# Kernel tuning notes

Hardware: AMD Instinct MI355X
Metric: run time of the kernel (lower is better)

Reference implementation:

```python
import jax, jax.numpy as jnp
import numpy as np

B, D, C = 8192, 1024, 4096  # batch, d_model, num_clusters (all active)
EPS = 1e-12  # matches F.normalize eps


def _l2_normalize(x):
    n = jnp.linalg.norm(x, axis=-1, keepdims=True)
    return x / jnp.maximum(n, EPS)


def setup_inputs() -> dict:
    key = jax.random.key(0)
    k1, k2 = jax.random.split(key)
    embedding = jax.random.normal(k1, (B, D), dtype=jnp.float32)
    centroids = jax.random.normal(k2, (C, D), dtype=jnp.float32)  # buffer, all active
    return {"embedding": embedding, "centroids": centroids}


def reference(embedding, centroids):
    # Fused equivalent of the per-centroid Python loop:
    # cosine sim of normalized embedding vs each normalized centroid.
    emb_n = _l2_normalize(embedding)        # [B, D]
    cen_n = _l2_normalize(centroids)        # [C, D]
    sims = jnp.clip(emb_n @ cen_n.T, 0.0, 1.0)  # [B, C], per-sim clamp to [0,1]
    max_sim = jnp.max(sims, axis=-1)        # [B]
    closest = jnp.argmax(sims, axis=-1)     # [B] int
    novelty = jnp.clip(jnp.sqrt(1.0 - max_sim), 0.0, 1.0)  # [B]
    return novelty, closest
```

## Files before the change

### kernel.cpp

```cpp
#include <hip/hip_runtime.h>
#include <math.h>

#define B_ROWS 8192
#define C_COLS 4096
#define D_DIM  1024
#define EPSN   1e-12f

typedef float v4f __attribute__((ext_vector_type(4)));
typedef short v8s __attribute__((ext_vector_type(8)));

__device__ __forceinline__ unsigned short bf16_rtn(float x) {
    unsigned int u = __float_as_uint(x);
    u += 0x7fffu + ((u >> 16) & 1u);
    return (unsigned short)(u >> 16);
}

__device__ __forceinline__ bool better_vi(float v, int i, float V, int I) {
    return (v > V) || (v == V && i < I);
}

__global__ __launch_bounds__(256) void prep_kernel(
    const float* __restrict__ emb, const float* __restrict__ cen,
    unsigned short* __restrict__ Ah, unsigned short* __restrict__ Bh,
    float* __restrict__ inv_a, float* __restrict__ inv_b)
{
    const int lane = threadIdx.x & 63;
    const int wid  = blockIdx.x * 4 + (threadIdx.x >> 6);
    const float* src; unsigned short* dst; float* invp; int r;
    if (wid < B_ROWS) { src = emb; r = wid;          dst = Ah; invp = inv_a; }
    else              { src = cen; r = wid - B_ROWS; dst = Bh; invp = inv_b; }

    const float* rp = src + (size_t)r * D_DIM;
    float4 v[4];
    float ss = 0.0f;
    #pragma unroll
    for (int j = 0; j < 4; ++j) {
        v[j] = *(const float4*)(rp + (j * 64 + lane) * 4);
        ss += v[j].x * v[j].x + v[j].y * v[j].y + v[j].z * v[j].z + v[j].w * v[j].w;
    }
    #pragma unroll
    for (int off = 1; off < 64; off <<= 1) ss += __shfl_xor(ss, off, 64);

    const float iv = 1.0f / fmaxf(sqrtf(ss), EPSN);
    if (lane == 0) invp[r] = iv;

    unsigned short* dp = dst + (size_t)r * D_DIM;
    #pragma unroll
    for (int j = 0; j < 4; ++j) {
        ushort4 H;
        H.x = bf16_rtn(v[j].x * iv);
        H.y = bf16_rtn(v[j].y * iv);
        H.z = bf16_rtn(v[j].z * iv);
        H.w = bf16_rtn(v[j].w * iv);
        *(ushort4*)(dp + (j * 64 + lane) * 4) = H;
    }
}

__global__ __launch_bounds__(256, 4) void simmax_kernel(
    const unsigned short* __restrict__ Ahg, const unsigned short* __restrict__ Bhg,
    float* __restrict__ p1v, int* __restrict__ p1i,
    float* __restrict__ p2v, int* __restrict__ p2i)
{
    __shared__ unsigned short lds[2 * 8192];

    const int tid    = threadIdx.x;
    const int L      = tid & 63;
    const int w      = tid >> 6;
    const int lane15 = L & 15;
    const int quad   = L >> 4;
    const int wr     = w >> 1, wc = w & 1;
    const int row0   = blockIdx.x * 128;
    const int c0     = blockIdx.y * 128;

    const int scol = (tid & 7) ^ ((tid >> 3) & 7);
    const unsigned short* aBase = Ahg + (size_t)(row0 + (tid >> 3)) * D_DIM + scol * 8;
    const unsigned short* bBase = Bhg + (size_t)(c0   + (tid >> 3)) * D_DIM + scol * 8;

    v4f acc[4][4];
    #pragma unroll
    for (int mt = 0; mt < 4; ++mt)
        #pragma unroll
        for (int nt = 0; nt < 4; ++nt) acc[mt][nt] = (v4f)0.0f;

    int rAo[4], rBo[4];
    #pragma unroll
    for (int t = 0; t < 4; ++t) {
        rAo[t] = (wr * 64 + t * 16 + lane15) * 64;
        rBo[t] = (wc * 64 + t * 16 + lane15) * 64;
    }
    const int s7 = lane15 & 7;
    const int cq[2] = { (quad ^ s7) * 8, ((4 + quad) ^ s7) * 8 };

    for (int kc = 0; kc < D_DIM / 64; ++kc) {
        const int kb = kc * 64;
        #pragma unroll
        for (int i = 0; i < 4; ++i) {
            __builtin_amdgcn_global_load_lds(
                (const __attribute__((address_space(1))) void*)(aBase + (size_t)i * 32 * D_DIM + kb),
                (__attribute__((address_space(3))) void*)&lds[(i * 256 + w * 64) * 8], 16, 0, 0);
            __builtin_amdgcn_global_load_lds(
                (const __attribute__((address_space(1))) void*)(bBase + (size_t)i * 32 * D_DIM + kb),
                (__attribute__((address_space(3))) void*)&lds[8192 + (i * 256 + w * 64) * 8], 16, 0, 0);
        }
        __syncthreads();

        #pragma unroll
        for (int h = 0; h < 2; ++h) {
            v8s fah[4], fbh[4];
            #pragma unroll
            for (int t = 0; t < 4; ++t) {
                fah[t] = *(const v8s*)&lds[rAo[t] + cq[h]];
                fbh[t] = *(const v8s*)&lds[8192 + rBo[t] + cq[h]];
            }
            #pragma unroll
            for (int mt = 0; mt < 4; ++mt)
                #pragma unroll
                for (int nt = 0; nt < 4; ++nt)
                    acc[mt][nt] = __builtin_amdgcn_mfma_f32_16x16x32_bf16(fah[mt], fbh[nt], acc[mt][nt], 0, 0, 0);
        }
        __syncthreads();
    }

    const int pc = blockIdx.y * 2 + wc;
    #pragma unroll
    for (int mt = 0; mt < 4; ++mt) {
        #pragma unroll
        for (int r = 0; r < 4; ++r) {
            float a1v = acc[mt][0][r];
            int   a1i = c0 + wc * 64 + 0 * 16 + lane15;
            float a2v = -1e30f;
            int   a2i = 0x7fffffff;
            #pragma unroll
            for (int nt = 1; nt < 4; ++nt) {
                float v  = acc[mt][nt][r];
                int   ci = c0 + wc * 64 + nt * 16 + lane15;
                if (better_vi(v, ci, a1v, a1i))      { a2v = a1v; a2i = a1i; a1v = v; a1i = ci; }
                else if (better_vi(v, ci, a2v, a2i)) { a2v = v;   a2i = ci; }
            }
            #pragma unroll
            for (int off = 8; off; off >>= 1) {
                float b1v = __shfl_down(a1v, off, 64); int b1i = __shfl_down(a1i, off, 64);
                float b2v = __shfl_down(a2v, off, 64); int b2i = __shfl_down(a2i, off, 64);
                if (better_vi(b1v, b1i, a1v, a1i)) {
                    if (better_vi(a1v, a1i, b2v, b2i)) { a2v = a1v; a2i = a1i; }
                    else                               { a2v = b2v; a2i = b2i; }
                    a1v = b1v; a1i = b1i;
                } else if (better_vi(b1v, b1i, a2v, a2i)) {
                    a2v = b1v; a2i = b1i;
                }
            }
            if (lane15 == 0) {
                int rg = row0 + wr * 64 + mt * 16 + quad * 4 + r;
                size_t ix = (size_t)rg * 64 + pc;
                p1v[ix] = a1v; p1i[ix] = a1i;
                p2v[ix] = a2v; p2i[ix] = a2i;
            }
        }
    }
}

__global__ __launch_bounds__(256) void finalize_kernel(
    const float* __restrict__ emb, const float* __restrict__ cen,
    const float* __restrict__ inv_a, const float* __restrict__ inv_b,
    const float* __restrict__ p1v, const int* __restrict__ p1i,
    const float* __restrict__ p2v, const int* __restrict__ p2i,
    float* __restrict__ out)
{
    const int lane = threadIdx.x & 63;
    const int row  = blockIdx.x * 4 + (threadIdx.x >> 6);
    const size_t base = (size_t)row * 64 + lane;

    float v[4]; int ix[4];
    v[0] = p1v[base]; ix[0] = p1i[base];
    v[1] = p2v[base]; ix[1] = p2i[base];
    v[2] = -1e30f;    ix[2] = 0x7ffffffe;
    v[3] = -1e30f;    ix[3] = 0x7fffffff;

    #pragma unroll
    for (int off = 1; off < 64; off <<= 1) {
        float ov[4]; int oi[4];
        #pragma unroll
        for (int k = 0; k < 4; ++k) {
            ov[k] = __shfl_xor(v[k],  off, 64);
            oi[k] = __shfl_xor(ix[k], off, 64);
        }
        #pragma unroll
        for (int k = 0; k < 4; ++k) {
            float bv = ov[k]; int bi = oi[k];
            bool b0 = better_vi(bv, bi, v[0], ix[0]);
            bool b1 = better_vi(bv, bi, v[1], ix[1]);
            bool b2 = better_vi(bv, bi, v[2], ix[2]);
            bool b3 = better_vi(bv, bi, v[3], ix[3]);
            float nv3 = b2 ? v[2] : (b3 ? bv : v[3]); int ni3 = b2 ? ix[2] : (b3 ? bi : ix[3]);
            float nv2 = b1 ? v[1] : (b2 ? bv : v[2]); int ni2 = b1 ? ix[1] : (b2 ? bi : ix[2]);
            float nv1 = b0 ? v[0] : (b1 ? bv : v[1]); int ni1 = b0 ? ix[0] : (b1 ? bi : ix[1]);
            float nv0 = b0 ? bv   : v[0];             int ni0 = b0 ? bi    : ix[0];
            v[0] = nv0; ix[0] = ni0; v[1] = nv1; ix[1] = ni1;
            v[2] = nv2; ix[2] = ni2; v[3] = nv3; ix[3] = ni3;
        }
    }

    const float* er = emb + (size_t)row * D_DIM;
    const float* cr0 = cen + (size_t)ix[0] * D_DIM;
    const float* cr1 = cen + (size_t)ix[1] * D_DIM;
    const float* cr2 = cen + (size_t)ix[2] * D_DIM;
    const float* cr3 = cen + (size_t)ix[3] * D_DIM;

    float d[4] = { 0.0f, 0.0f, 0.0f, 0.0f };
    #pragma unroll
    for (int j = 0; j < 4; ++j) {
        int e = (j * 64 + lane) * 4;
        float4 ev = *(const float4*)(er  + e);
        float4 c0 = *(const float4*)(cr0 + e);
        float4 c1 = *(const float4*)(cr1 + e);
        float4 c2 = *(const float4*)(cr2 + e);
        float4 c3 = *(const float4*)(cr3 + e);
        d[0] += ev.x * c0.x + ev.y * c0.y + ev.z * c0.z + ev.w * c0.w;
        d[1] += ev.x * c1.x + ev.y * c1.y + ev.z * c1.z + ev.w * c1.w;
        d[2] += ev.x * c2.x + ev.y * c2.y + ev.z * c2.z + ev.w * c2.w;
        d[3] += ev.x * c3.x + ev.y * c3.y + ev.z * c3.z + ev.w * c3.w;
    }
    #pragma unroll
    for (int off = 1; off < 64; off <<= 1) {
        #pragma unroll
        for (int c = 0; c < 4; ++c) d[c] += __shfl_xor(d[c], off, 64);
    }

    if (lane == 0) {
        const float ia = inv_a[row];
        float m = -1e30f; int ci = 0x7fffffff;
        #pragma unroll
        for (int c = 0; c < 4; ++c) {
            float s = d[c] * ia * inv_b[ix[c]];
            if (better_vi(s, ix[c], m, ci)) { m = s; ci = ix[c]; }
        }
        if (m <= 0.0f) ci = 0;
        float ms = fminf(fmaxf(m, 0.0f), 1.0f);
        out[row]          = fminf(fmaxf(sqrtf(1.0f - ms), 0.0f), 1.0f);
        out[B_ROWS + row] = (float)ci;
    }
}

extern "C" void kernel_launch(void* const* d_in, const int* in_sizes, int n_in,
                              void* d_out, int out_size, void* d_ws, size_t ws_size,
                              hipStream_t stream)
{
    const float* emb = (const float*)d_in[0];
    const float* cen = (const float*)d_in[1];
    float* out = (float*)d_out;

    unsigned short* Ahp = (unsigned short*)d_ws;
    unsigned short* Bhp = Ahp + (size_t)B_ROWS * D_DIM;
    float* inv_a = (float*)(Bhp + (size_t)C_COLS * D_DIM);
    float* inv_b = inv_a + B_ROWS;
    float* p1v   = inv_b + C_COLS;
    int*   p1i   = (int*)(p1v + (size_t)64 * B_ROWS);
    float* p2v   = (float*)(p1i + (size_t)64 * B_ROWS);
    int*   p2i   = (int*)(p2v + (size_t)64 * B_ROWS);

    prep_kernel<<<(B_ROWS + C_COLS) / 4, 256, 0, stream>>>(emb, cen, Ahp, Bhp, inv_a, inv_b);

    dim3 grid(B_ROWS / 128, C_COLS / 128);
    simmax_kernel<<<grid, 256, 0, stream>>>(Ahp, Bhp, p1v, p1i, p2v, p2i);

    finalize_kernel<<<B_ROWS / 4, 256, 0, stream>>>(emb, cen, inv_a, inv_b,
                                                    p1v, p1i, p2v, p2i, out);
}
```

Baseline: 207.8 us.

## Triple-buffer GEMM loads with 512-thread 128x256 tiles and split MFMA phases

The similarity GEMM moves from 128x128 tiles with 4 waves and a single-buffered load/sync loop to 128x256 tiles with 8 waves. Global-to-LDS loads go into a three-stage ring buffer, with the prefetch for step t+2 issued in two halves interleaved with two MFMA phases. Explicit vmcnt waits, barriers and s_setprio hints are meant to hide load latency and raise MFMA utilization. In exchange it uses much more LDS (about 144 KB per block) and fewer resident blocks, and the partial-result indexing now depends on the wider column tiles.

```diff
diff --git a/kernel.cpp b/kernel.cpp
--- a/kernel.cpp
+++ b/kernel.cpp
@@ -56,25 +56,43 @@
     }
 }
 
-__global__ __launch_bounds__(256, 4) void simmax_kernel(
+#define GLD16(gp, lp) \
+    __builtin_amdgcn_global_load_lds( \
+        (const __attribute__((address_space(1))) void*)(gp), \
+        (__attribute__((address_space(3))) void*)(lp), 16, 0, 0)
+
+__global__ __launch_bounds__(512, 2) void simmax_kernel(
     const unsigned short* __restrict__ Ahg, const unsigned short* __restrict__ Bhg,
     float* __restrict__ p1v, int* __restrict__ p1i,
     float* __restrict__ p2v, int* __restrict__ p2i)
 {
-    __shared__ unsigned short lds[2 * 8192];
+    __shared__ unsigned short lds[3 * 24576];
 
     const int tid    = threadIdx.x;
     const int L      = tid & 63;
     const int w      = tid >> 6;
     const int lane15 = L & 15;
     const int quad   = L >> 4;
-    const int wr     = w >> 1, wc = w & 1;
+    const int wr     = w >> 2;
+    const int wc     = w & 3;
     const int row0   = blockIdx.x * 128;
-    const int c0     = blockIdx.y * 128;
+    const int c0     = blockIdx.y * 256;
 
     const int scol = (tid & 7) ^ ((tid >> 3) & 7);
-    const unsigned short* aBase = Ahg + (size_t)(row0 + (tid >> 3)) * D_DIM + scol * 8;
-    const unsigned short* bBase = Bhg + (size_t)(c0   + (tid >> 3)) * D_DIM + scol * 8;
+    const unsigned short* aB = Ahg + (size_t)(row0 + (tid >> 3)) * D_DIM + scol * 8;
+    const unsigned short* bB = Bhg + (size_t)(c0   + (tid >> 3)) * D_DIM + scol * 8;
+    const int wofs = w * 512;
+
+#define STAGE3A(bo, kb) do { \
+    GLD16(aB + (kb),           &lds[(bo) + wofs]);           \
+    GLD16(aB + 65536 + (kb),   &lds[(bo) + 4096  + wofs]);   \
+    GLD16(bB + (kb),           &lds[(bo) + 8192  + wofs]);   \
+} while (0)
+#define STAGE3B(bo, kb) do { \
+    GLD16(bB + 65536 + (kb),   &lds[(bo) + 12288 + wofs]);   \
+    GLD16(bB + 131072 + (kb),  &lds[(bo) + 16384 + wofs]);   \
+    GLD16(bB + 196608 + (kb),  &lds[(bo) + 20480 + wofs]);   \
+} while (0)
 
     v4f acc[4][4];
     #pragma unroll
@@ -86,42 +104,79 @@
     #pragma unroll
     for (int t = 0; t < 4; ++t) {
         rAo[t] = (wr * 64 + t * 16 + lane15) * 64;
-        rBo[t] = (wc * 64 + t * 16 + lane15) * 64;
-    }
-    const int s7 = lane15 & 7;
-    const int cq[2] = { (quad ^ s7) * 8, ((4 + quad) ^ s7) * 8 };
-
-    for (int kc = 0; kc < D_DIM / 64; ++kc) {
-        const int kb = kc * 64;
-        #pragma unroll
-        for (int i = 0; i < 4; ++i) {
-            __builtin_amdgcn_global_load_lds(
-                (const __attribute__((address_space(1))) void*)(aBase + (size_t)i * 32 * D_DIM + kb),
-                (__attribute__((address_space(3))) void*)&lds[(i * 256 + w * 64) * 8], 16, 0, 0);
-            __builtin_amdgcn_global_load_lds(
-                (const __attribute__((address_space(1))) void*)(bBase + (size_t)i * 32 * D_DIM + kb),
-                (__attribute__((address_space(3))) void*)&lds[8192 + (i * 256 + w * 64) * 8], 16, 0, 0);
-        }
-        __syncthreads();
-
-        #pragma unroll
-        for (int h = 0; h < 2; ++h) {
-            v8s fah[4], fbh[4];
+        rBo[t] = 8192 + (wc * 64 + t * 16 + lane15) * 64;
+    }
+    const int s7  = lane15 & 7;
+    const int cq0 = (quad ^ s7) * 8;
+    const int cq1 = ((4 + quad) ^ s7) * 8;
+
+    STAGE3A(0, 0);      STAGE3B(0, 0);
+    STAGE3A(24576, 64); STAGE3B(24576, 64);
+    asm volatile("s_waitcnt vmcnt(6)" ::: "memory");
+    __builtin_amdgcn_s_barrier();
+
+    int bo_c = 0, bo_n = 24576, bo_n2 = 49152;
+    for (int t = 0; t < 16; ++t) {
+        const bool pf  = (t + 2 < 16);
+        const int  kb2 = (t + 2) * 64;
+
+        v8s fb[4][2], fa[2][2];
+        #pragma unroll
+        for (int nt = 0; nt < 4; ++nt) {
+            fb[nt][0] = *(const v8s*)&lds[bo_c + rBo[nt] + cq0];
+            fb[nt][1] = *(const v8s*)&lds[bo_c + rBo[nt] + cq1];
+        }
+        #pragma unroll
+        for (int mt = 0; mt < 2; ++mt) {
+            fa[mt][0] = *(const v8s*)&lds[bo_c + rAo[mt] + cq0];
+            fa[mt][1] = *(const v8s*)&lds[bo_c + rAo[mt] + cq1];
+        }
+        if (pf) STAGE3A(bo_n2, kb2);
+        __builtin_amdgcn_s_barrier();
+        asm volatile("s_waitcnt lgkmcnt(0)" ::: "memory");
+        __builtin_amdgcn_sched_barrier(0);
+        __builtin_amdgcn_s_setprio(1);
+        #pragma unroll
+        for (int kk = 0; kk < 2; ++kk)
             #pragma unroll
-            for (int t = 0; t < 4; ++t) {
-                fah[t] = *(const v8s*)&lds[rAo[t] + cq[h]];
-                fbh[t] = *(const v8s*)&lds[8192 + rBo[t] + cq[h]];
-            }
-            #pragma unroll
-            for (int mt = 0; mt < 4; ++mt)
+            for (int mt = 0; mt < 2; ++mt)
                 #pragma unroll
                 for (int nt = 0; nt < 4; ++nt)
-                    acc[mt][nt] = __builtin_amdgcn_mfma_f32_16x16x32_bf16(fah[mt], fbh[nt], acc[mt][nt], 0, 0, 0);
-        }
-        __syncthreads();
-    }
-
-    const int pc = blockIdx.y * 2 + wc;
+                    acc[mt][nt] = __builtin_amdgcn_mfma_f32_16x16x32_bf16(
+                        fa[mt][kk], fb[nt][kk], acc[mt][nt], 0, 0, 0);
+        __builtin_amdgcn_s_setprio(0);
+        __builtin_amdgcn_s_barrier();
+
+        v8s fa2[2][2];
+        #pragma unroll
+        for (int mt = 0; mt < 2; ++mt) {
+            fa2[mt][0] = *(const v8s*)&lds[bo_c + rAo[2 + mt] + cq0];
+            fa2[mt][1] = *(const v8s*)&lds[bo_c + rAo[2 + mt] + cq1];
+        }
+        if (pf) STAGE3B(bo_n2, kb2);
+        __builtin_amdgcn_s_barrier();
+        asm volatile("s_waitcnt lgkmcnt(0)" ::: "memory");
+        __builtin_amdgcn_sched_barrier(0);
+        __builtin_amdgcn_s_setprio(1);
+        #pragma unroll
+        for (int kk = 0; kk < 2; ++kk)
+            #pragma unroll
+            for (int mt = 0; mt < 2; ++mt)
+                #pragma unroll
+                for (int nt = 0; nt < 4; ++nt)
+                    acc[2 + mt][nt] = __builtin_amdgcn_mfma_f32_16x16x32_bf16(
+                        fa2[mt][kk], fb[nt][kk], acc[2 + mt][nt], 0, 0, 0);
+        __builtin_amdgcn_s_setprio(0);
+
+        if (t < 15) {
+            if (pf) asm volatile("s_waitcnt vmcnt(6)" ::: "memory");
+            else    asm volatile("s_waitcnt vmcnt(0)" ::: "memory");
+            __builtin_amdgcn_s_barrier();
+        }
+        const int tb = bo_c; bo_c = bo_n; bo_n = bo_n2; bo_n2 = tb;
+    }
+
+    const int pc = blockIdx.y * 4 + wc;
     #pragma unroll
     for (int mt = 0; mt < 4; ++mt) {
         #pragma unroll
@@ -260,8 +315,8 @@
 
     prep_kernel<<<(B_ROWS + C_COLS) / 4, 256, 0, stream>>>(emb, cen, Ahp, Bhp, inv_a, inv_b);
 
-    dim3 grid(B_ROWS / 128, C_COLS / 128);
-    simmax_kernel<<<grid, 256, 0, stream>>>(Ahp, Bhp, p1v, p1i, p2v, p2i);
+    dim3 grid(B_ROWS / 128, C_COLS / 256);
+    simmax_kernel<<<grid, 512, 0, stream>>>(Ahp, Bhp, p1v, p1i, p2v, p2i);
 
     finalize_kernel<<<B_ROWS / 4, 256, 0, stream>>>(emb, cen, inv_a, inv_b,
                                                     p1v, p1i, p2v, p2i, out);
```

After: 232.1 us. 1.12x slower.

## Enlarge GEMM tile to 256x256 with double-buffered LDS and swizzled block order

Applied to the files above, without the earlier changes.

The similarity GEMM kernel moves from 128x128 tiles with 4 waves to 256x256 tiles with 8 waves per block, each wave computing a 128x64 sub-tile. The K loop is now double-buffered in LDS so the next chunk's global-to-LDS loads are issued before the current chunk's MFMAs, which also removes one barrier per iteration. Block IDs are remapped into grouped tiles to improve L2 locality. The partial-argmax column index layout still yields 64 partials per row. Costs are 128KB of LDS and 128 accumulator registers per thread, which may limit occupancy.

```diff
diff --git a/kernel.cpp b/kernel.cpp
--- a/kernel.cpp
+++ b/kernel.cpp
@@ -56,74 +56,94 @@
     }
 }
 
-__global__ __launch_bounds__(256, 4) void simmax_kernel(
+#define GLD16(gp, lp) \
+    __builtin_amdgcn_global_load_lds( \
+        (const __attribute__((address_space(1))) void*)(gp), \
+        (__attribute__((address_space(3))) void*)(lp), 16, 0, 0)
+
+__global__ __launch_bounds__(512, 2) void simmax_kernel(
     const unsigned short* __restrict__ Ahg, const unsigned short* __restrict__ Bhg,
     float* __restrict__ p1v, int* __restrict__ p1i,
     float* __restrict__ p2v, int* __restrict__ p2i)
 {
-    __shared__ unsigned short lds[2 * 8192];
+    __shared__ unsigned short lds[2 * 32768];
 
     const int tid    = threadIdx.x;
     const int L      = tid & 63;
     const int w      = tid >> 6;
     const int lane15 = L & 15;
     const int quad   = L >> 4;
-    const int wr     = w >> 1, wc = w & 1;
-    const int row0   = blockIdx.x * 128;
-    const int c0     = blockIdx.y * 128;
+    const int wr     = w >> 2;
+    const int wc     = w & 3;
+
+    const int bid = blockIdx.x;
+    const int c   = bid & 7, s = bid >> 3;
+    const int gx  = ((c & 3) << 3) + (s & 7);
+    const int gy  = ((c >> 2) << 3) + (s >> 3);
+    const int row0 = gx * 256;
+    const int c0   = gy * 256;
 
     const int scol = (tid & 7) ^ ((tid >> 3) & 7);
-    const unsigned short* aBase = Ahg + (size_t)(row0 + (tid >> 3)) * D_DIM + scol * 8;
-    const unsigned short* bBase = Bhg + (size_t)(c0   + (tid >> 3)) * D_DIM + scol * 8;
-
-    v4f acc[4][4];
-    #pragma unroll
-    for (int mt = 0; mt < 4; ++mt)
+    const unsigned short* aB = Ahg + (size_t)(row0 + (tid >> 3)) * D_DIM + scol * 8;
+    const unsigned short* bB = Bhg + (size_t)(c0   + (tid >> 3)) * D_DIM + scol * 8;
+    const int wofs = w * 512;
+
+#define STAGE_ALL(bo, kb) do { \
+    GLD16(aB + (kb),           &lds[(bo) + 0     + wofs]); \
+    GLD16(aB + 65536  + (kb),  &lds[(bo) + 4096  + wofs]); \
+    GLD16(aB + 131072 + (kb),  &lds[(bo) + 8192  + wofs]); \
+    GLD16(aB + 196608 + (kb),  &lds[(bo) + 12288 + wofs]); \
+    GLD16(bB + (kb),           &lds[(bo) + 16384 + wofs]); \
+    GLD16(bB + 65536  + (kb),  &lds[(bo) + 20480 + wofs]); \
+    GLD16(bB + 131072 + (kb),  &lds[(bo) + 24576 + wofs]); \
+    GLD16(bB + 196608 + (kb),  &lds[(bo) + 28672 + wofs]); \
+} while (0)
+
+    v4f acc[8][4];
+    #pragma unroll
+    for (int mt = 0; mt < 8; ++mt)
         #pragma unroll
         for (int nt = 0; nt < 4; ++nt) acc[mt][nt] = (v4f)0.0f;
 
-    int rAo[4], rBo[4];
-    #pragma unroll
-    for (int t = 0; t < 4; ++t) {
-        rAo[t] = (wr * 64 + t * 16 + lane15) * 64;
-        rBo[t] = (wc * 64 + t * 16 + lane15) * 64;
-    }
-    const int s7 = lane15 & 7;
-    const int cq[2] = { (quad ^ s7) * 8, ((4 + quad) ^ s7) * 8 };
-
-    for (int kc = 0; kc < D_DIM / 64; ++kc) {
-        const int kb = kc * 64;
-        #pragma unroll
-        for (int i = 0; i < 4; ++i) {
-            __builtin_amdgcn_global_load_lds(
-                (const __attribute__((address_space(1))) void*)(aBase + (size_t)i * 32 * D_DIM + kb),
-                (__attribute__((address_space(3))) void*)&lds[(i * 256 + w * 64) * 8], 16, 0, 0);
-            __builtin_amdgcn_global_load_lds(
-                (const __attribute__((address_space(1))) void*)(bBase + (size_t)i * 32 * D_DIM + kb),
-                (__attribute__((address_space(3))) void*)&lds[8192 + (i * 256 + w * 64) * 8], 16, 0, 0);
-        }
-        __syncthreads();
+    int rA[8], rB[4];
+    #pragma unroll
+    for (int t = 0; t < 8; ++t) rA[t] = (wr * 128 + t * 16 + lane15) * 64;
+    #pragma unroll
+    for (int t = 0; t < 4; ++t) rB[t] = 16384 + (wc * 64 + t * 16 + lane15) * 64;
+    const int s7  = lane15 & 7;
+    const int cq0 = (quad ^ s7) * 8;
+    const int cq1 = ((4 + quad) ^ s7) * 8;
+
+    STAGE_ALL(0, 0);
+    __syncthreads();
+
+    int cur = 0;
+    for (int t = 0; t < 16; ++t) {
+        const int bo = cur << 15;
+        if (t < 15) STAGE_ALL(32768 - bo, (t + 1) * 64);
 
         #pragma unroll
         for (int h = 0; h < 2; ++h) {
-            v8s fah[4], fbh[4];
-            #pragma unroll
-            for (int t = 0; t < 4; ++t) {
-                fah[t] = *(const v8s*)&lds[rAo[t] + cq[h]];
-                fbh[t] = *(const v8s*)&lds[8192 + rBo[t] + cq[h]];
-            }
-            #pragma unroll
-            for (int mt = 0; mt < 4; ++mt)
+            const int cq = h ? cq1 : cq0;
+            v8s fb[4], fa[8];
+            #pragma unroll
+            for (int nt = 0; nt < 4; ++nt) fb[nt] = *(const v8s*)&lds[bo + rB[nt] + cq];
+            #pragma unroll
+            for (int mt = 0; mt < 8; ++mt) fa[mt] = *(const v8s*)&lds[bo + rA[mt] + cq];
+            #pragma unroll
+            for (int mt = 0; mt < 8; ++mt)
                 #pragma unroll
                 for (int nt = 0; nt < 4; ++nt)
-                    acc[mt][nt] = __builtin_amdgcn_mfma_f32_16x16x32_bf16(fah[mt], fbh[nt], acc[mt][nt], 0, 0, 0);
-        }
-        __syncthreads();
-    }
-
-    const int pc = blockIdx.y * 2 + wc;
-    #pragma unroll
-    for (int mt = 0; mt < 4; ++mt) {
+                    acc[mt][nt] = __builtin_amdgcn_mfma_f32_16x16x32_bf16(
+                        fa[mt], fb[nt], acc[mt][nt], 0, 0, 0);
+        }
+        if (t < 15) __syncthreads();
+        cur ^= 1;
+    }
+
+    const int pc = gy * 4 + wc;
+    #pragma unroll
+    for (int mt = 0; mt < 8; ++mt) {
         #pragma unroll
         for (int r = 0; r < 4; ++r) {
             float a1v = acc[mt][0][r];
@@ -150,7 +170,7 @@
                 }
             }
             if (lane15 == 0) {
-                int rg = row0 + wr * 64 + mt * 16 + quad * 4 + r;
+                int rg = row0 + wr * 128 + mt * 16 + quad * 4 + r;
                 size_t ix = (size_t)rg * 64 + pc;
                 p1v[ix] = a1v; p1i[ix] = a1i;
                 p2v[ix] = a2v; p2i[ix] = a2i;
@@ -260,8 +280,7 @@
 
     prep_kernel<<<(B_ROWS + C_COLS) / 4, 256, 0, stream>>>(emb, cen, Ahp, Bhp, inv_a, inv_b);
 
-    dim3 grid(B_ROWS / 128, C_COLS / 128);
-    simmax_kernel<<<grid, 256, 0, stream>>>(Ahp, Bhp, p1v, p1i, p2v, p2i);
+    simmax_kernel<<<dim3(512), 512, 0, stream>>>(Ahp, Bhp, p1v, p1i, p2v, p2i);
 
     finalize_kernel<<<B_ROWS / 4, 256, 0, stream>>>(emb, cen, inv_a, inv_b,
                                                     p1v, p1i, p2v, p2i, out);
```

After: 222.5 us. 1.07x slower.

## Enlarge GEMM block tile to 256x128 with 512 threads sharing B tile

Applied to the files above, without the earlier changes.

Doubles the row dimension of each simmax block to 256 rows using 8 waves, so each staged centroid tile in LDS is reused by twice as many waves. The staging code is rewritten so each thread issues six 16-byte global-to-LDS loads per K-chunk, and LDS grows to 48KB. This is meant to cut global/L2 traffic for the B operand and halve the block count. In exchange, larger blocks and more LDS per block may lower occupancy. The epilogue's per-wave indexing of partial results must also still line up with the new wave layout.

```diff
diff --git a/kernel.cpp b/kernel.cpp
--- a/kernel.cpp
+++ b/kernel.cpp
@@ -56,25 +56,41 @@
     }
 }
 
-__global__ __launch_bounds__(256, 4) void simmax_kernel(
+#define GLD16(gp, lp) \
+    __builtin_amdgcn_global_load_lds( \
+        (const __attribute__((address_space(1))) void*)(gp), \
+        (__attribute__((address_space(3))) void*)(lp), 16, 0, 0)
+
+__global__ __launch_bounds__(512, 4) void simmax_kernel(
     const unsigned short* __restrict__ Ahg, const unsigned short* __restrict__ Bhg,
     float* __restrict__ p1v, int* __restrict__ p1i,
     float* __restrict__ p2v, int* __restrict__ p2i)
 {
-    __shared__ unsigned short lds[2 * 8192];
+    __shared__ unsigned short lds[24576];
 
     const int tid    = threadIdx.x;
     const int L      = tid & 63;
     const int w      = tid >> 6;
     const int lane15 = L & 15;
     const int quad   = L >> 4;
-    const int wr     = w >> 1, wc = w & 1;
-    const int row0   = blockIdx.x * 128;
+    const int wr     = w >> 1;
+    const int wc     = w & 1;
+    const int row0   = blockIdx.x * 256;
     const int c0     = blockIdx.y * 128;
 
     const int scol = (tid & 7) ^ ((tid >> 3) & 7);
-    const unsigned short* aBase = Ahg + (size_t)(row0 + (tid >> 3)) * D_DIM + scol * 8;
-    const unsigned short* bBase = Bhg + (size_t)(c0   + (tid >> 3)) * D_DIM + scol * 8;
+    const unsigned short* aB = Ahg + (size_t)(row0 + (tid >> 3)) * D_DIM + scol * 8;
+    const unsigned short* bB = Bhg + (size_t)(c0   + (tid >> 3)) * D_DIM + scol * 8;
+    const int wofs = w * 512;
+
+#define STAGE_ALL(kb) do { \
+    GLD16(aB + (kb),           &lds[0     + wofs]); \
+    GLD16(aB + 65536  + (kb),  &lds[4096  + wofs]); \
+    GLD16(aB + 131072 + (kb),  &lds[8192  + wofs]); \
+    GLD16(aB + 196608 + (kb),  &lds[12288 + wofs]); \
+    GLD16(bB + (kb),           &lds[16384 + wofs]); \
+    GLD16(bB + 65536  + (kb),  &lds[20480 + wofs]); \
+} while (0)
 
     v4f acc[4][4];
     #pragma unroll
@@ -86,22 +102,13 @@
     #pragma unroll
     for (int t = 0; t < 4; ++t) {
         rAo[t] = (wr * 64 + t * 16 + lane15) * 64;
-        rBo[t] = (wc * 64 + t * 16 + lane15) * 64;
+        rBo[t] = 16384 + (wc * 64 + t * 16 + lane15) * 64;
     }
     const int s7 = lane15 & 7;
     const int cq[2] = { (quad ^ s7) * 8, ((4 + quad) ^ s7) * 8 };
 
     for (int kc = 0; kc < D_DIM / 64; ++kc) {
-        const int kb = kc * 64;
-        #pragma unroll
-        for (int i = 0; i < 4; ++i) {
-            __builtin_amdgcn_global_load_lds(
-                (const __attribute__((address_space(1))) void*)(aBase + (size_t)i * 32 * D_DIM + kb),
-                (__attribute__((address_space(3))) void*)&lds[(i * 256 + w * 64) * 8], 16, 0, 0);
-            __builtin_amdgcn_global_load_lds(
-                (const __attribute__((address_space(1))) void*)(bBase + (size_t)i * 32 * D_DIM + kb),
-                (__attribute__((address_space(3))) void*)&lds[8192 + (i * 256 + w * 64) * 8], 16, 0, 0);
-        }
+        STAGE_ALL(kc * 64);
         __syncthreads();
 
         #pragma unroll
@@ -110,13 +117,14 @@
             #pragma unroll
             for (int t = 0; t < 4; ++t) {
                 fah[t] = *(const v8s*)&lds[rAo[t] + cq[h]];
-                fbh[t] = *(const v8s*)&lds[8192 + rBo[t] + cq[h]];
+                fbh[t] = *(const v8s*)&lds[rBo[t] + cq[h]];
             }
             #pragma unroll
             for (int mt = 0; mt < 4; ++mt)
                 #pragma unroll
                 for (int nt = 0; nt < 4; ++nt)
-                    acc[mt][nt] = __builtin_amdgcn_mfma_f32_16x16x32_bf16(fah[mt], fbh[nt], acc[mt][nt], 0, 0, 0);
+                    acc[mt][nt] = __builtin_amdgcn_mfma_f32_16x16x32_bf16(
+                        fah[mt], fbh[nt], acc[mt][nt], 0, 0, 0);
         }
         __syncthreads();
     }
@@ -260,8 +268,8 @@
 
     prep_kernel<<<(B_ROWS + C_COLS) / 4, 256, 0, stream>>>(emb, cen, Ahp, Bhp, inv_a, inv_b);
 
-    dim3 grid(B_ROWS / 128, C_COLS / 128);
-    simmax_kernel<<<grid, 256, 0, stream>>>(Ahp, Bhp, p1v, p1i, p2v, p2i);
+    dim3 grid(B_ROWS / 256, C_COLS / 128);
+    simmax_kernel<<<grid, 512, 0, stream>>>(Ahp, Bhp, p1v, p1i, p2v, p2i);
 
     finalize_kernel<<<B_ROWS / 4, 256, 0, stream>>>(emb, cen, inv_a, inv_b,
                                                     p1v, p1i, p2v, p2i, out);
```

Result: faster. 198.9 us (-4.3%).
